# Optimization experiments

Measured on AMD Instinct MI355X. Metric: run time of the kernel, lower is better.

The kernel has to match this reference:

```python
import jax, jax.numpy as jnp
import numpy as np

D_IN = 768
D_SAE = 768 * 16  # expansion_factor = 16
K = 64
BATCH = 8192


def setup_inputs() -> dict:
    key = jax.random.key(0)
    k1, k2, k3 = jax.random.split(key, 3)
    x = jax.random.normal(k1, (BATCH, D_IN), dtype=jnp.float32)
    # Kaiming-uniform-ish encoder init (exact init values don't matter for correctness)
    bound = (6.0 / D_IN) ** 0.5
    W_enc = jax.random.uniform(k2, (D_IN, D_SAE), dtype=jnp.float32, minval=-bound, maxval=bound)
    b_enc = jnp.zeros((D_SAE,), dtype=jnp.float32)
    W_dec = jax.random.normal(k3, (D_SAE, D_IN), dtype=jnp.float32) * (1.0 / D_IN ** 0.5)
    # unit-norm decoder rows (per the module's normalize_decoder_weights)
    W_dec = W_dec / (jnp.linalg.norm(W_dec, axis=1, keepdims=True) + 1e-8)
    b_dec = jnp.zeros((D_IN,), dtype=jnp.float32)
    return {"x": x, "W_enc": W_enc, "b_enc": b_enc, "W_dec": W_dec, "b_dec": b_dec}


def reference(x, W_enc, b_enc, W_dec, b_dec):
    # encode: center, dense matmul, ReLU
    pre_acts = jax.nn.relu((x - b_dec) @ W_enc + b_enc)  # [B, d_sae]
    # top-k selection per row, scatter back into dense sparse_acts
    topk_vals, topk_idx = jax.lax.top_k(pre_acts, K)  # [B, K]
    rows = jnp.arange(pre_acts.shape[0])[:, None]  # [B, 1]
    sparse_acts = jnp.zeros_like(pre_acts).at[rows, topk_idx].set(topk_vals)
    # decode: dense matmul + bias
    reconstruction = sparse_acts @ W_dec + b_dec  # [B, d_in]
    return (reconstruction, sparse_acts)
```

## Files before the change

kernel.cpp:

```cpp
#include <hip/hip_runtime.h>
#include <hip/hip_fp16.h>
#include <stdint.h>

#define D_IN   768
#define D_SAE  12288
#define BATCH  8192
#define K_TOP  64
#define CAND_MAX 256

typedef _Float16 f16;
typedef _Float16 v8h __attribute__((ext_vector_type(8)));
typedef float v4f __attribute__((ext_vector_type(4)));

__device__ inline void async16(const void* g, void* l) {
    __builtin_amdgcn_global_load_lds(
        (const __attribute__((address_space(1))) unsigned int*)g,
        (__attribute__((address_space(3))) unsigned int*)l, 16, 0, 0);
}

__global__ __launch_bounds__(256) void k_convert_x(
    const float* __restrict__ x, const float* __restrict__ b_dec,
    f16* __restrict__ xhi, f16* __restrict__ xlo)
{
    int i4 = (blockIdx.x * 256 + threadIdx.x) * 4;
    float4 v = *(const float4*)(x + i4);
    int col = i4 % D_IN;
    float vv[4] = { v.x - b_dec[col], v.y - b_dec[col + 1],
                    v.z - b_dec[col + 2], v.w - b_dec[col + 3] };
    union { short4 s; f16 h[4]; } H, L;
#pragma unroll
    for (int u = 0; u < 4; ++u) {
        H.h[u] = (f16)vv[u];
        L.h[u] = (f16)(vv[u] - (float)H.h[u]);
    }
    *(short4*)(xhi + i4) = H.s;
    *(short4*)(xlo + i4) = L.s;
}

__global__ __launch_bounds__(256) void k_convert_wt(
    const float* __restrict__ W, f16* __restrict__ whiT, f16* __restrict__ wloT)
{
    __shared__ float tile[32][33];
    const int n0 = blockIdx.x * 32;
    const int k0 = blockIdx.y * 32;
    const int c = threadIdx.x & 31;
    const int rr = threadIdx.x >> 5;
#pragma unroll
    for (int s = 0; s < 4; ++s) {
        int r = s * 8 + rr;
        tile[r][c] = W[(size_t)(k0 + r) * D_SAE + n0 + c];
    }
    __syncthreads();
#pragma unroll
    for (int s = 0; s < 4; ++s) {
        int r2 = s * 8 + rr;
        float v = tile[c][r2];
        f16 hi = (f16)v;
        f16 lo = (f16)(v - (float)hi);
        whiT[(size_t)(n0 + r2) * D_IN + k0 + c] = hi;
        wloT[(size_t)(n0 + r2) * D_IN + k0 + c] = lo;
    }
}

__global__ __launch_bounds__(256) void k_gemm_f16(
    const f16* __restrict__ A,
    const f16* __restrict__ Bt,
    const float* __restrict__ b_enc,
    f16* __restrict__ outap)
{
    __shared__ f16 Asm[2][128 * 32];
    __shared__ f16 Bsm[2][128 * 32];
    const int tid  = threadIdx.x;
    const int wave = tid >> 6;
    const int lane = tid & 63;
    const int bn = blockIdx.x * 128;
    const int bm = blockIdx.y * 128;

    const int r16  = lane >> 2;
    const int kc8  = (lane & 3) * 8;
    const int mrow = lane & 15;
    const int quad = lane >> 4;
    const int wm = (wave & 1) * 64;
    const int wn = (wave >> 1) * 64;

    v4f acc[4][4] = {};

    const f16* gA = A  + (size_t)(bm + wave * 32 + r16) * D_IN + kc8;
    const f16* gB = Bt + (size_t)(bn + wave * 32 + r16) * D_IN + kc8;
    f16* lA0  = &Asm[0][(wave * 32) * 32];
    f16* lA0b = &Asm[0][(wave * 32 + 16) * 32];
    f16* lB0  = &Bsm[0][(wave * 32) * 32];
    f16* lB0b = &Bsm[0][(wave * 32 + 16) * 32];
    f16* lA1  = &Asm[1][(wave * 32) * 32];
    f16* lA1b = &Asm[1][(wave * 32 + 16) * 32];
    f16* lB1  = &Bsm[1][(wave * 32) * 32];
    f16* lB1b = &Bsm[1][(wave * 32 + 16) * 32];

    for (int k0 = 0; k0 < D_IN; k0 += 64) {
        __syncthreads();
        async16(gA + k0,               lA0);
        async16(gA + k0 + 16 * D_IN,   lA0b);
        async16(gB + k0,               lB0);
        async16(gB + k0 + 16 * D_IN,   lB0b);
        async16(gA + k0 + 32,              lA1);
        async16(gA + k0 + 32 + 16 * D_IN,  lA1b);
        async16(gB + k0 + 32,              lB1);
        async16(gB + k0 + 32 + 16 * D_IN,  lB1b);
        __syncthreads();

#pragma unroll
        for (int s = 0; s < 2; ++s) {
            v8h af[4], bf[4];
#pragma unroll
            for (int i = 0; i < 4; ++i)
                af[i] = *(const v8h*)&Asm[s][(wm + i * 16 + mrow) * 32 + quad * 8];
#pragma unroll
            for (int j = 0; j < 4; ++j)
                bf[j] = *(const v8h*)&Bsm[s][(wn + j * 16 + mrow) * 32 + quad * 8];
#pragma unroll
            for (int i = 0; i < 4; ++i)
#pragma unroll
                for (int j = 0; j < 4; ++j)
                    acc[i][j] = __builtin_amdgcn_mfma_f32_16x16x32_f16(af[i], bf[j], acc[i][j], 0, 0, 0);
        }
    }

#pragma unroll
    for (int i = 0; i < 4; ++i) {
#pragma unroll
        for (int r = 0; r < 4; ++r) {
            int grow = bm + wm + i * 16 + quad * 4 + r;
            f16* op = outap + (size_t)grow * (2 * D_SAE) + bn + wn;
#pragma unroll
            for (int j = 0; j < 4; ++j) {
                int c = j * 16 + mrow;
                float val = acc[i][j][r] + b_enc[bn + wn + c];
                __builtin_nontemporal_store((f16)(val > 0.f ? val : 0.f), op + c);
            }
        }
    }
}

__global__ __launch_bounds__(256) void k_topk2(
    float* __restrict__ sparse,
    const f16* __restrict__ Xhi, const f16* __restrict__ Xlo,
    const f16* __restrict__ WhiT, const f16* __restrict__ WloT,
    const float* __restrict__ b_enc,
    const float* __restrict__ Wdec,
    const float* __restrict__ b_dec,
    float* __restrict__ recon)
{
    const int row = blockIdx.x;
    const int t = threadIdx.x;
    float* rp = sparse + (size_t)row * D_SAE;
    const f16* ap = (const f16*)rp;

    v8h av[6];
#pragma unroll
    for (int j = 0; j < 6; ++j)
        av[j] = __builtin_nontemporal_load((const v8h*)(ap + ((size_t)j * 256 + t) * 8));

    __shared__ unsigned hist[256];
    __shared__ unsigned suf[256];
    __shared__ float sh_cutoff;
    __shared__ int sh_ncand;
    __shared__ int   cand_i[CAND_MAX];
    __shared__ float cand_v[CAND_MAX];
    __shared__ float kept_v[K_TOP];
    __shared__ int   kept_i[K_TOP];
    __shared__ float xr[D_IN];

    const float margin = 0.05f;

    hist[t] = 0;
    if (t == 0) sh_ncand = 0;
    __syncthreads();
#pragma unroll
    for (int j = 0; j < 6; ++j)
#pragma unroll
        for (int u = 0; u < 8; ++u) {
            float x = (float)av[j][u];
            if (x >= 0.25f) {
                int b = (int)(x * 32.0f); if (b > 255) b = 255;
                atomicAdd(&hist[b], 1u);
            }
        }
    __syncthreads();
    suf[t] = hist[t];
    __syncthreads();
    for (int off = 1; off < 256; off <<= 1) {
        unsigned add = (t + off < 256) ? suf[t + off] : 0u;
        __syncthreads();
        suf[t] += add;
        __syncthreads();
    }
    unsigned total0 = suf[0];
    if (total0 >= K_TOP) {
        if (suf[t] >= K_TOP && (t == 255 || suf[t + 1] < K_TOP))
            sh_cutoff = fmaxf((float)t * (1.0f / 32.0f) - margin, 1e-30f);
    } else {
        __syncthreads();
        hist[t] = 0;
        __syncthreads();
#pragma unroll
        for (int j = 0; j < 6; ++j)
#pragma unroll
            for (int u = 0; u < 8; ++u) {
                float x = (float)av[j][u];
                if (x > 0.0f && x < 0.25f) {
                    int b = (int)(x * 1024.0f); if (b > 255) b = 255;
                    atomicAdd(&hist[b], 1u);
                }
            }
        __syncthreads();
        suf[t] = hist[t];
        __syncthreads();
        for (int off = 1; off < 256; off <<= 1) {
            unsigned add = (t + off < 256) ? suf[t + off] : 0u;
            __syncthreads();
            suf[t] += add;
            __syncthreads();
        }
        unsigned need = K_TOP - total0;
        if (suf[0] >= need) {
            if (suf[t] >= need && (t == 255 || suf[t + 1] < need))
                sh_cutoff = fmaxf((float)t * (1.0f / 1024.0f) - margin, 1e-30f);
        } else {
            if (t == 0) sh_cutoff = 1e-30f;
        }
    }
    __syncthreads();
    const float cutoff = sh_cutoff;

#pragma unroll
    for (int j = 0; j < 6; ++j)
#pragma unroll
        for (int u = 0; u < 8; ++u) {
            float x = (float)av[j][u];
            if (x >= cutoff) {
                int pos = atomicAdd(&sh_ncand, 1);
                if (pos < CAND_MAX) { cand_i[pos] = (j * 256 + t) * 8 + u; cand_v[pos] = x; }
            }
        }
    __syncthreads();
    int ncand = sh_ncand; if (ncand > CAND_MAX) ncand = CAND_MAX;

    for (int k = t; k < D_IN; k += 256)
        xr[k] = (float)Xhi[(size_t)row * D_IN + k] + (float)Xlo[(size_t)row * D_IN + k];
    __syncthreads();
    for (int c = t; c < ncand; c += 256) {
        const f16* wh = WhiT + (size_t)cand_i[c] * D_IN;
        const f16* wl = WloT + (size_t)cand_i[c] * D_IN;
        float acc = 0.f;
        for (int k = 0; k < D_IN; k += 8) {
            v8h hv = *(const v8h*)(wh + k);
            v8h lv = *(const v8h*)(wl + k);
#pragma unroll
            for (int u = 0; u < 8; ++u)
                acc += xr[k + u] * ((float)hv[u] + (float)lv[u]);
        }
        acc += b_enc[cand_i[c]];
        cand_v[c] = acc > 0.f ? acc : 0.f;
    }
    __syncthreads();

    for (int c = t; c < ncand; c += 256) {
        float vc = cand_v[c]; int ic = cand_i[c];
        int r = 0;
        for (int m = 0; m < ncand; ++m) {
            float vm = cand_v[m];
            r += (vm > vc || (vm == vc && cand_i[m] < ic)) ? 1 : 0;
        }
        if (r < K_TOP) { kept_v[r] = vc; kept_i[r] = ic; }
    }
    __syncthreads();
    int nk = ncand < K_TOP ? ncand : K_TOP;

#pragma unroll
    for (int j = 0; j < 12; ++j) {
        v4f z = {0.f, 0.f, 0.f, 0.f};
        __builtin_nontemporal_store(z, (v4f*)(rp + ((size_t)j * 256 + t) * 4));
    }
    __syncthreads();
    if (t < nk) rp[kept_i[t]] = kept_v[t];

    float r0 = b_dec[t], r1 = b_dec[t + 256], r2 = b_dec[t + 512];
    for (int m = 0; m < nk; ++m) {
        float val = kept_v[m];
        const float* wr = Wdec + (size_t)kept_i[m] * D_IN;
        r0 += val * wr[t];
        r1 += val * wr[t + 256];
        r2 += val * wr[t + 512];
    }
    float* rc = recon + (size_t)row * D_IN;
    __builtin_nontemporal_store(r0, rc + t);
    __builtin_nontemporal_store(r1, rc + t + 256);
    __builtin_nontemporal_store(r2, rc + t + 512);
}

extern "C" void kernel_launch(void* const* d_in, const int* in_sizes, int n_in,
                              void* d_out, int out_size, void* d_ws, size_t ws_size,
                              hipStream_t stream) {
    const float* x     = (const float*)d_in[0];
    const float* W_enc = (const float*)d_in[1];
    const float* b_enc = (const float*)d_in[2];
    const float* W_dec = (const float*)d_in[3];
    const float* b_dec = (const float*)d_in[4];
    float* out    = (float*)d_out;
    float* recon  = out;
    float* sparse = out + (size_t)BATCH * D_IN;

    const size_t xplane = (size_t)BATCH * D_IN;
    const size_t wplane = (size_t)D_SAE * D_IN;
    f16* xhi  = (f16*)d_ws;
    f16* xlo  = xhi + xplane;
    f16* whiT = xlo + xplane;
    f16* wloT = whiT + wplane;

    k_convert_x<<<xplane / 1024, 256, 0, stream>>>(x, b_dec, xhi, xlo);
    k_convert_wt<<<dim3(D_SAE / 32, D_IN / 32), 256, 0, stream>>>(W_enc, whiT, wloT);
    k_gemm_f16<<<dim3(D_SAE / 128, BATCH / 128), 256, 0, stream>>>(xhi, whiT, b_enc, (f16*)sparse);
    k_topk2<<<BATCH, 256, 0, stream>>>(sparse, xhi, xlo, whiT, wloT, b_enc, W_dec, b_dec, recon);
}
```

Measured before the change: 1.237 ms.

## Restructure top-k selection with wave-level scans, ballot compaction, and early zeroing

Replaces the 256-step shared-memory suffix scan, which needed many barriers, with a wave-shuffle scan plus a 4-entry cross-wave combine. Candidate insertion now uses ballot-based aggregated atomics instead of one atomic per element. A coarse histogram tier for values at or above 2.0 is added, so the common case can find its cutoff with fewer candidates. The row-zeroing stores and the x reload are moved earlier to overlap with the selection work, and the decode loop is unrolled. The early zeroing depends on an explicit vmcnt wait so the loads finish before the buffer is overwritten, and the extra tier adds another histogram pass whenever fewer than K values reach 2.0.

```diff
diff --git a/kernel.cpp b/kernel.cpp
--- a/kernel.cpp
+++ b/kernel.cpp
@@ -141,6 +141,28 @@
     }
 }
 
+__device__ __forceinline__ unsigned suffix_scan_256(unsigned h, int t, unsigned* wtot, unsigned* tot_out) {
+    const int lane = t & 63;
+    const int w = t >> 6;
+    unsigned s = h;
+#pragma unroll
+    for (int off = 1; off < 64; off <<= 1) {
+        unsigned o = __shfl_down(s, off);
+        if (lane + off < 64) s += o;
+    }
+    if (lane == 0) wtot[w] = s;
+    __syncthreads();
+    unsigned suf = s;
+    unsigned tot = 0;
+#pragma unroll
+    for (int w2 = 0; w2 < 4; ++w2) {
+        tot += wtot[w2];
+        if (w2 > w) suf += wtot[w2];
+    }
+    *tot_out = tot;
+    return suf;
+}
+
 __global__ __launch_bounds__(256) void k_topk2(
     float* __restrict__ sparse,
     const f16* __restrict__ Xhi, const f16* __restrict__ Xlo,
@@ -152,6 +174,7 @@
 {
     const int row = blockIdx.x;
     const int t = threadIdx.x;
+    const int lane = t & 63;
     float* rp = sparse + (size_t)row * D_SAE;
     const f16* ap = (const f16*)rp;
 
@@ -160,8 +183,15 @@
     for (int j = 0; j < 6; ++j)
         av[j] = __builtin_nontemporal_load((const v8h*)(ap + ((size_t)j * 256 + t) * 8));
 
+    asm volatile("s_waitcnt vmcnt(0)" ::: "memory");
+#pragma unroll
+    for (int j = 0; j < 12; ++j) {
+        v4f z = {0.f, 0.f, 0.f, 0.f};
+        __builtin_nontemporal_store(z, (v4f*)(rp + ((size_t)j * 256 + t) * 4));
+    }
+
     __shared__ unsigned hist[256];
-    __shared__ unsigned suf[256];
+    __shared__ unsigned wtot[4];
     __shared__ float sh_cutoff;
     __shared__ int sh_ncand;
     __shared__ int   cand_i[CAND_MAX];
@@ -174,32 +204,30 @@
 
     hist[t] = 0;
     if (t == 0) sh_ncand = 0;
-    __syncthreads();
+    for (int k = t; k < D_IN; k += 256)
+        xr[k] = (float)Xhi[(size_t)row * D_IN + k] + (float)Xlo[(size_t)row * D_IN + k];
+    __syncthreads();
+
 #pragma unroll
     for (int j = 0; j < 6; ++j)
 #pragma unroll
         for (int u = 0; u < 8; ++u) {
             float x = (float)av[j][u];
-            if (x >= 0.25f) {
-                int b = (int)(x * 32.0f); if (b > 255) b = 255;
+            if (x >= 2.0f) {
+                int b = (int)((x - 2.0f) * 32.0f); if (b > 255) b = 255;
                 atomicAdd(&hist[b], 1u);
             }
         }
     __syncthreads();
-    suf[t] = hist[t];
-    __syncthreads();
-    for (int off = 1; off < 256; off <<= 1) {
-        unsigned add = (t + off < 256) ? suf[t + off] : 0u;
-        __syncthreads();
-        suf[t] += add;
-        __syncthreads();
-    }
-    unsigned total0 = suf[0];
-    if (total0 >= K_TOP) {
-        if (suf[t] >= K_TOP && (t == 255 || suf[t + 1] < K_TOP))
-            sh_cutoff = fmaxf((float)t * (1.0f / 32.0f) - margin, 1e-30f);
-    } else {
-        __syncthreads();
+    unsigned h0 = hist[t];
+    unsigned tot0;
+    unsigned suf0 = suffix_scan_256(h0, t, wtot, &tot0);
+    if (tot0 >= K_TOP) {
+        if (suf0 >= K_TOP && suf0 - h0 < K_TOP)
+            sh_cutoff = fmaxf(2.0f + (float)t * (1.0f / 32.0f) - margin, 1e-30f);
+    }
+    __syncthreads();
+    if (tot0 < K_TOP) {
         hist[t] = 0;
         __syncthreads();
 #pragma unroll
@@ -207,26 +235,44 @@
 #pragma unroll
             for (int u = 0; u < 8; ++u) {
                 float x = (float)av[j][u];
-                if (x > 0.0f && x < 0.25f) {
-                    int b = (int)(x * 1024.0f); if (b > 255) b = 255;
+                if (x >= 0.25f) {
+                    int b = (int)(x * 32.0f); if (b > 255) b = 255;
                     atomicAdd(&hist[b], 1u);
                 }
             }
         __syncthreads();
-        suf[t] = hist[t];
-        __syncthreads();
-        for (int off = 1; off < 256; off <<= 1) {
-            unsigned add = (t + off < 256) ? suf[t + off] : 0u;
+        unsigned h1 = hist[t];
+        unsigned tot1;
+        unsigned suf1 = suffix_scan_256(h1, t, wtot, &tot1);
+        if (tot1 >= K_TOP) {
+            if (suf1 >= K_TOP && suf1 - h1 < K_TOP)
+                sh_cutoff = fmaxf((float)t * (1.0f / 32.0f) - margin, 1e-30f);
+        }
+        __syncthreads();
+        if (tot1 < K_TOP) {
+            hist[t] = 0;
             __syncthreads();
-            suf[t] += add;
+#pragma unroll
+            for (int j = 0; j < 6; ++j)
+#pragma unroll
+                for (int u = 0; u < 8; ++u) {
+                    float x = (float)av[j][u];
+                    if (x > 0.0f && x < 0.25f) {
+                        int b = (int)(x * 1024.0f); if (b > 255) b = 255;
+                        atomicAdd(&hist[b], 1u);
+                    }
+                }
             __syncthreads();
-        }
-        unsigned need = K_TOP - total0;
-        if (suf[0] >= need) {
-            if (suf[t] >= need && (t == 255 || suf[t + 1] < need))
-                sh_cutoff = fmaxf((float)t * (1.0f / 1024.0f) - margin, 1e-30f);
-        } else {
-            if (t == 0) sh_cutoff = 1e-30f;
+            unsigned h2 = hist[t];
+            unsigned tot2;
+            unsigned suf2 = suffix_scan_256(h2, t, wtot, &tot2);
+            unsigned need = K_TOP - tot1;
+            if (tot2 >= need) {
+                if (suf2 >= need && suf2 - h2 < need)
+                    sh_cutoff = fmaxf((float)t * (1.0f / 1024.0f) - margin, 1e-30f);
+            } else {
+                if (t == 0) sh_cutoff = 1e-30f;
+            }
         }
     }
     __syncthreads();
@@ -237,17 +283,23 @@
 #pragma unroll
         for (int u = 0; u < 8; ++u) {
             float x = (float)av[j][u];
-            if (x >= cutoff) {
-                int pos = atomicAdd(&sh_ncand, 1);
-                if (pos < CAND_MAX) { cand_i[pos] = (j * 256 + t) * 8 + u; cand_v[pos] = x; }
+            bool pass = (x >= cutoff);
+            unsigned long long m = __ballot(pass);
+            if (m != 0ull) {
+                int leader = (int)__builtin_ctzll(m);
+                int cnt = (int)__builtin_popcountll(m);
+                int base0 = 0;
+                if (lane == leader) base0 = atomicAdd(&sh_ncand, cnt);
+                base0 = __shfl(base0, leader);
+                if (pass) {
+                    int pos = base0 + (int)__builtin_popcountll(m & ((1ull << lane) - 1ull));
+                    if (pos < CAND_MAX) { cand_i[pos] = (j * 256 + t) * 8 + u; cand_v[pos] = x; }
+                }
             }
         }
     __syncthreads();
     int ncand = sh_ncand; if (ncand > CAND_MAX) ncand = CAND_MAX;
 
-    for (int k = t; k < D_IN; k += 256)
-        xr[k] = (float)Xhi[(size_t)row * D_IN + k] + (float)Xlo[(size_t)row * D_IN + k];
-    __syncthreads();
     for (int c = t; c < ncand; c += 256) {
         const f16* wh = WhiT + (size_t)cand_i[c] * D_IN;
         const f16* wl = WloT + (size_t)cand_i[c] * D_IN;
@@ -276,15 +328,10 @@
     __syncthreads();
     int nk = ncand < K_TOP ? ncand : K_TOP;
 
-#pragma unroll
-    for (int j = 0; j < 12; ++j) {
-        v4f z = {0.f, 0.f, 0.f, 0.f};
-        __builtin_nontemporal_store(z, (v4f*)(rp + ((size_t)j * 256 + t) * 4));
-    }
-    __syncthreads();
     if (t < nk) rp[kept_i[t]] = kept_v[t];
 
     float r0 = b_dec[t], r1 = b_dec[t + 256], r2 = b_dec[t + 512];
+#pragma unroll 4
     for (int m = 0; m < nk; ++m) {
         float val = kept_v[m];
         const float* wr = Wdec + (size_t)kept_i[m] * D_IN;
```

After: 1.245 ms. Within noise of the previous version (+0.7%).
